# Kernel tuning notes

Hardware: AMD Instinct MI355X
Metric: run time of the kernel (lower is better)

Reference implementation:

```python
import jax, jax.numpy as jnp
import numpy as np

EPS = 1e-5


def gcn_conv(x, W, b, src, dst, ew, num_nodes):
    """GCNConv with add_self_loops=True, symmetric normalization (PyG default)."""
    # degree at destination, self-loop weight 1.0 included implicitly
    deg = jax.ops.segment_sum(ew, dst, num_segments=num_nodes) + 1.0  # [N]
    dinv = jax.lax.rsqrt(deg)                                         # deg >= 1
    norm = dinv[src] * ew * dinv[dst]                                 # [E]
    h = x @ W                                                         # [N, F]
    msg = norm[:, None] * h[src]                                      # [E, F]
    agg = jax.ops.segment_sum(msg, dst, num_segments=num_nodes)       # [N, F]
    # self-loop contribution: dinv[i] * 1 * dinv[i] = 1/deg[i]
    agg = agg + h * (1.0 / deg)[:, None]
    return agg + b


def batchnorm(h, gamma, beta):
    mean = jnp.mean(h, axis=0)
    var = jnp.mean(jnp.square(h - mean), axis=0)  # biased, training-mode stats
    return (h - mean) * jax.lax.rsqrt(var + EPS) * gamma + beta


def setup_inputs() -> dict:
    key = jax.random.key(0)
    ks = jax.random.split(key, 8)
    N, E, F = 50000, 800000, 64
    x = jax.random.normal(ks[0], (N, F), dtype=jnp.float32)
    edge_index = jax.random.randint(ks[1], (2, E), 0, N, dtype=jnp.int64)
    edge_weight = jax.random.uniform(ks[2], (E,), dtype=jnp.float32)
    s = 1.0 / np.sqrt(F)
    W1 = jax.random.uniform(ks[3], (F, F), jnp.float32, -s, s)
    b1 = jnp.zeros((F,), jnp.float32)
    W2 = jax.random.uniform(ks[4], (F, F), jnp.float32, -s, s)
    b2 = jnp.zeros((F,), jnp.float32)
    gamma1 = jnp.ones((F,), jnp.float32)
    beta1 = jnp.zeros((F,), jnp.float32)
    gamma2 = jnp.ones((F,), jnp.float32)
    beta2 = jnp.zeros((F,), jnp.float32)
    return {"x": x, "edge_index": edge_index, "edge_weight": edge_weight,
            "W1": W1, "b1": b1, "gamma1": gamma1, "beta1": beta1,
            "W2": W2, "b2": b2, "gamma2": gamma2, "beta2": beta2}


def reference(x, edge_index, edge_weight, W1, b1, gamma1, beta1, W2, b2, gamma2, beta2):
    N = x.shape[0]
    src, dst = edge_index[0], edge_index[1]
    identity = x
    out = gcn_conv(x, W1, b1, src, dst, edge_weight, N)
    out = jax.nn.relu(batchnorm(out, gamma1, beta1))
    out = gcn_conv(out, W2, b2, src, dst, edge_weight, N)
    out = batchnorm(out, gamma2, beta2)
    out = out + identity  # residual: num_input_features == hidden_dim
    return jax.nn.relu(out)
```

## Files before the change

### kernel.cpp

```cpp
#include <hip/hip_runtime.h>
#include <math.h>

#define FEAT 64
#define BN_EPS 1e-5f

__device__ __forceinline__ int edge_idx(const void* p, int is64, long long i) {
    return is64 ? (int)((const long long*)p)[i] : ((const int*)p)[i];
}

__device__ __forceinline__ float4 f4fma(float a, float4 b, float4 c) {
    return make_float4(fmaf(a, b.x, c.x), fmaf(a, b.y, c.y),
                       fmaf(a, b.z, c.z), fmaf(a, b.w, c.w));
}

__device__ __forceinline__ unsigned bf16rtne(float f) {
    unsigned u = __float_as_uint(f);
    return (u + 0x7fffu + ((u >> 16) & 1u)) >> 16;
}
__device__ __forceinline__ unsigned packbf2(float a, float b) {
    return bf16rtne(a) | (bf16rtne(b) << 16);
}
__device__ __forceinline__ float4 unpackbf4(uint2 r) {
    return make_float4(__uint_as_float(r.x << 16),
                       __uint_as_float(r.x & 0xffff0000u),
                       __uint_as_float(r.y << 16),
                       __uint_as_float(r.y & 0xffff0000u));
}

__global__ __launch_bounds__(256) void init_kernel(
    const unsigned* __restrict__ w, int* __restrict__ flag,
    int* __restrict__ cnt, float* __restrict__ parts, int N) {
    int i = blockIdx.x * 256 + threadIdx.x;
    if (i < N) cnt[i] = 0;
    if (blockIdx.x < 8) parts[blockIdx.x * 256 + threadIdx.x] = 0.0f;
    if (blockIdx.x == 0 && threadIdx.x < 64) {
        unsigned long long ok = __ballot(w[2 * threadIdx.x + 1] == 0u);
        if (threadIdx.x == 0) *flag = (ok == ~0ull);
    }
}

__global__ __launch_bounds__(256) void count_seq_kernel(
    const void* __restrict__ ei, const int* __restrict__ flag,
    int* __restrict__ cnt, int* __restrict__ seq, int E) {
    int is64 = *flag;
    int T = gridDim.x * 256;
    int i = blockIdx.x * 256 + threadIdx.x;
#pragma unroll
    for (int u = 0; u < 8; ++u) {
        int e = i + u * T;
        if (e < E) {
            int dst = edge_idx(ei, is64, (long long)E + e);
            seq[e] = atomicAdd(&cnt[dst], 1);
        }
    }
}

__global__ __launch_bounds__(256) void scan1_kernel(const int* __restrict__ cnt,
                                                    int* __restrict__ excl,
                                                    int* __restrict__ bsum, int N) {
    __shared__ int tmp[256];
    int i = blockIdx.x * 256 + threadIdx.x;
    int v = (i < N) ? cnt[i] : 0;
    tmp[threadIdx.x] = v;
    __syncthreads();
    for (int off = 1; off < 256; off <<= 1) {
        int t = (threadIdx.x >= off) ? tmp[threadIdx.x - off] : 0;
        __syncthreads();
        tmp[threadIdx.x] += t;
        __syncthreads();
    }
    if (i < N) excl[i] = tmp[threadIdx.x] - v;
    if (threadIdx.x == 255) bsum[blockIdx.x] = tmp[255];
}

__global__ __launch_bounds__(256) void scan2_kernel(int* __restrict__ bsum, int nb) {
    __shared__ int tmp[256];
    int i = threadIdx.x;
    int v = (i < nb) ? bsum[i] : 0;
    tmp[i] = v;
    __syncthreads();
    for (int off = 1; off < 256; off <<= 1) {
        int t = (i >= off) ? tmp[i - off] : 0;
        __syncthreads();
        tmp[i] += t;
        __syncthreads();
    }
    if (i < nb) bsum[i] = tmp[i] - v;
}

__global__ void scan3_kernel(const int* __restrict__ excl,
                             const int* __restrict__ bsum,
                             int* __restrict__ rowptr, int N, int E) {
    int i = blockIdx.x * 256 + threadIdx.x;
    if (i < N) rowptr[i] = excl[i] + bsum[blockIdx.x];
    if (i == 0) rowptr[N] = E;
}

__global__ __launch_bounds__(256) void scatter_csr_kernel(
    const void* __restrict__ ei, const float* __restrict__ ew,
    const int* __restrict__ flag, const int* __restrict__ rowptr,
    const int* __restrict__ seq, int2* __restrict__ csr, int E) {
    int is64 = *flag;
    int T = gridDim.x * 256;
    int i = blockIdx.x * 256 + threadIdx.x;
#pragma unroll
    for (int u = 0; u < 2; ++u) {
        int e = i + u * T;
        if (e < E) {
            int src = edge_idx(ei, is64, e);
            int dst = edge_idx(ei, is64, (long long)E + e);
            int pos = rowptr[dst] + seq[e];
            csr[pos] = make_int2(src, __float_as_int(ew[e]));
        }
    }
}

__global__ __launch_bounds__(256) void deg_inv_kernel(
    const int* __restrict__ rowptr, const int2* __restrict__ csr,
    float* __restrict__ dinv, float* __restrict__ invdeg, int N) {
    int t = blockIdx.x * 256 + threadIdx.x;
    int n = t >> 3, l = t & 7;
    if (n >= N) return;
    int b = rowptr[n], e = rowptr[n + 1];
    float d = 0.0f;
    for (int k = b + l; k < e; k += 8) d += __int_as_float(csr[k].y);
    d += __shfl_xor(d, 1);
    d += __shfl_xor(d, 2);
    d += __shfl_xor(d, 4);
    if (l == 0) {
        d += 1.0f;
        dinv[n]   = rsqrtf(d);
        invdeg[n] = 1.0f / d;
    }
}

__global__ __launch_bounds__(256) void fold_kernel(int2* __restrict__ csr,
                                                   const float* __restrict__ dinv,
                                                   int E) {
    int T = gridDim.x * 256;
    int i = blockIdx.x * 256 + threadIdx.x;
#pragma unroll
    for (int u = 0; u < 2; ++u) {
        int e = i + u * T;
        if (e < E) {
            int2 v = csr[e];
            csr[e].y = __float_as_int(dinv[v.x] * __int_as_float(v.y));
        }
    }
}

__global__ __launch_bounds__(256) void gemm64_kernel(
    const float* __restrict__ in, const float* __restrict__ W,
    const float* __restrict__ scale, const float* __restrict__ shift,
    uint2* __restrict__ out_bf, int N, int affine) {
    __shared__ float4 Ws4[64][16];
    __shared__ float xs[64][65];
    __shared__ float sA[64], sS[64];
    int tid = threadIdx.x;
    const float4* W4 = (const float4*)W;
    for (int j = tid; j < 1024; j += 256) Ws4[j >> 4][j & 15] = W4[j];
    if (affine && tid < 64) { sA[tid] = scale[tid]; sS[tid] = shift[tid]; }
    __syncthreads();

    int rowBase = blockIdx.x * 64;
    for (int j = tid; j < 1024; j += 256) {
        int r = j >> 4, q = j & 15;
        int row = rowBase + r;
        float4 v = make_float4(0.f, 0.f, 0.f, 0.f);
        if (row < N) {
            v = ((const float4*)in)[(size_t)row * 16 + q];
            if (affine) {
                int c = q * 4;
                v.x = fmaxf(fmaf(v.x, sA[c + 0], sS[c + 0]), 0.f);
                v.y = fmaxf(fmaf(v.y, sA[c + 1], sS[c + 1]), 0.f);
                v.z = fmaxf(fmaf(v.z, sA[c + 2], sS[c + 2]), 0.f);
                v.w = fmaxf(fmaf(v.w, sA[c + 3], sS[c + 3]), 0.f);
            }
        }
        xs[r][q * 4 + 0] = v.x;
        xs[r][q * 4 + 1] = v.y;
        xs[r][q * 4 + 2] = v.z;
        xs[r][q * 4 + 3] = v.w;
    }
    __syncthreads();

    int q = tid & 15, rg = tid >> 4;
    int r0 = rg * 4;
    float4 a0 = make_float4(0.f, 0.f, 0.f, 0.f), a1 = a0, a2 = a0, a3 = a0;
#pragma unroll 4
    for (int k = 0; k < 64; ++k) {
        float4 wv = Ws4[k][q];
        a0 = f4fma(xs[r0 + 0][k], wv, a0);
        a1 = f4fma(xs[r0 + 1][k], wv, a1);
        a2 = f4fma(xs[r0 + 2][k], wv, a2);
        a3 = f4fma(xs[r0 + 3][k], wv, a3);
    }
    int row = rowBase + r0;
    if (row + 0 < N) out_bf[(size_t)(row + 0) * 16 + q] = make_uint2(packbf2(a0.x, a0.y), packbf2(a0.z, a0.w));
    if (row + 1 < N) out_bf[(size_t)(row + 1) * 16 + q] = make_uint2(packbf2(a1.x, a1.y), packbf2(a1.z, a1.w));
    if (row + 2 < N) out_bf[(size_t)(row + 2) * 16 + q] = make_uint2(packbf2(a2.x, a2.y), packbf2(a2.z, a2.w));
    if (row + 3 < N) out_bf[(size_t)(row + 3) * 16 + q] = make_uint2(packbf2(a3.x, a3.y), packbf2(a3.z, a3.w));
}

__global__ __launch_bounds__(256) void gather_agg_kernel(
    const uint2* __restrict__ h2, const int* __restrict__ rowptr,
    const int2* __restrict__ csr, const float* __restrict__ dinv,
    const float* __restrict__ invdeg, const float* __restrict__ bias,
    float* __restrict__ agg, float* __restrict__ parts, int N) {
    int tid = threadIdx.x;
    int wave = tid >> 6, lane = tid & 63;
    int sub = lane >> 4, sl = lane & 15;
    float4 bv = ((const float4*)bias)[sl];
    float4 bnS = make_float4(0.f, 0.f, 0.f, 0.f), bnQ = bnS;

    for (int n = blockIdx.x * 4 + wave; n < N; n += gridDim.x * 4) {
        int beg = rowptr[n], end = rowptr[n + 1];
        float4 accE = make_float4(0.f, 0.f, 0.f, 0.f);
        int k = beg + sub;
        for (; k + 4 < end; k += 8) {
            int2 e0 = csr[k];
            int2 e1 = csr[k + 4];
            float4 h0 = unpackbf4(h2[(size_t)e0.x * 16 + sl]);
            float4 h1 = unpackbf4(h2[(size_t)e1.x * 16 + sl]);
            accE = f4fma(__int_as_float(e0.y), h0, accE);
            accE = f4fma(__int_as_float(e1.y), h1, accE);
        }
        if (k < end) {
            int2 e0 = csr[k];
            float4 h0 = unpackbf4(h2[(size_t)e0.x * 16 + sl]);
            accE = f4fma(__int_as_float(e0.y), h0, accE);
        }
        accE.x += __shfl_xor(accE.x, 16); accE.y += __shfl_xor(accE.y, 16);
        accE.z += __shfl_xor(accE.z, 16); accE.w += __shfl_xor(accE.w, 16);
        accE.x += __shfl_xor(accE.x, 32); accE.y += __shfl_xor(accE.y, 32);
        accE.z += __shfl_xor(accE.z, 32); accE.w += __shfl_xor(accE.w, 32);

        if (sub == 0) {
            float4 self = unpackbf4(h2[(size_t)n * 16 + sl]);
            float4 tot = f4fma(invdeg[n], self, bv);
            tot = f4fma(dinv[n], accE, tot);
            ((float4*)agg)[(size_t)n * 16 + sl] = tot;
            bnS.x += tot.x; bnS.y += tot.y; bnS.z += tot.z; bnS.w += tot.w;
            bnQ.x = fmaf(tot.x, tot.x, bnQ.x); bnQ.y = fmaf(tot.y, tot.y, bnQ.y);
            bnQ.z = fmaf(tot.z, tot.z, bnQ.z); bnQ.w = fmaf(tot.w, tot.w, bnQ.w);
        }
    }

    __shared__ float4 LS[4][16], LQ[4][16];
    if (sub == 0) { LS[wave][sl] = bnS; LQ[wave][sl] = bnQ; }
    __syncthreads();
    if (tid < 16) {
        float4 ts = LS[0][tid], tq = LQ[0][tid];
        for (int i = 1; i < 4; ++i) {
            float4 a = LS[i][tid], b = LQ[i][tid];
            ts.x += a.x; ts.y += a.y; ts.z += a.z; ts.w += a.w;
            tq.x += b.x; tq.y += b.y; tq.z += b.z; tq.w += b.w;
        }
        float* P = parts + (size_t)(blockIdx.x & 7) * 128;
        int c = tid * 4;
        unsafeAtomicAdd(&P[c + 0], ts.x);      unsafeAtomicAdd(&P[c + 1], ts.y);
        unsafeAtomicAdd(&P[c + 2], ts.z);      unsafeAtomicAdd(&P[c + 3], ts.w);
        unsafeAtomicAdd(&P[64 + c + 0], tq.x); unsafeAtomicAdd(&P[64 + c + 1], tq.y);
        unsafeAtomicAdd(&P[64 + c + 2], tq.z); unsafeAtomicAdd(&P[64 + c + 3], tq.w);
    }
}

__global__ void bn_final_kernel(const float* __restrict__ parts,
                                const float* __restrict__ gamma,
                                const float* __restrict__ beta,
                                float* __restrict__ a, float* __restrict__ s,
                                float invN) {
    int c = threadIdx.x;
    if (c < 64) {
        float sm = 0.f, sq = 0.f;
#pragma unroll
        for (int r = 0; r < 8; ++r) {
            sm += parts[r * 128 + c];
            sq += parts[r * 128 + 64 + c];
        }
        float m = sm * invN;
        float var = fmaxf(sq * invN - m * m, 0.0f);
        float aa = gamma[c] * rsqrtf(var + BN_EPS);
        a[c] = aa;
        s[c] = beta[c] - m * aa;
    }
}

__global__ void final_out_kernel(const float* __restrict__ agg,
                                 const float* __restrict__ a,
                                 const float* __restrict__ s,
                                 const float* __restrict__ x,
                                 float* __restrict__ out, int nquads) {
    int gid = blockIdx.x * 256 + threadIdx.x;
    if (gid < nquads) {
        int q = gid & 15;
        float4 av = ((const float4*)a)[q], sv = ((const float4*)s)[q];
        float4 g = ((const float4*)agg)[gid], xv = ((const float4*)x)[gid];
        float4 o;
        o.x = fmaxf(fmaf(g.x, av.x, sv.x) + xv.x, 0.f);
        o.y = fmaxf(fmaf(g.y, av.y, sv.y) + xv.y, 0.f);
        o.z = fmaxf(fmaf(g.z, av.z, sv.z) + xv.z, 0.f);
        o.w = fmaxf(fmaf(g.w, av.w, sv.w) + xv.w, 0.f);
        ((float4*)out)[gid] = o;
    }
}

extern "C" void kernel_launch(void* const* d_in, const int* in_sizes, int n_in,
                              void* d_out, int out_size, void* d_ws, size_t ws_size,
                              hipStream_t stream) {
    const float* x      = (const float*)d_in[0];
    const void*  ei     = d_in[1];
    const float* ew     = (const float*)d_in[2];
    const float* W1     = (const float*)d_in[3];
    const float* b1     = (const float*)d_in[4];
    const float* gamma1 = (const float*)d_in[5];
    const float* beta1  = (const float*)d_in[6];
    const float* W2     = (const float*)d_in[7];
    const float* b2     = (const float*)d_in[8];
    const float* gamma2 = (const float*)d_in[9];
    const float* beta2  = (const float*)d_in[10];
    float* out = (float*)d_out;

    const int N = in_sizes[0] / FEAT;
    const int E = in_sizes[2];

    char* ws = (char*)d_ws;
    size_t off = 0;
    auto alloc = [&](size_t bytes) {
        size_t o = off;
        off += (bytes + 255) & ~(size_t)255;
        return (void*)(ws + o);
    };
    int*   flag   = (int*)  alloc(256);
    int*   cnt    = (int*)  alloc((size_t)N * 4);
    int*   rowptr = (int*)  alloc((size_t)(N + 1) * 4);
    int*   seq    = (int*)  alloc((size_t)E * 4);
    int*   excl   = (int*)  alloc((size_t)N * 4);
    int*   bsum   = (int*)  alloc(256 * 4);
    float* dinv   = (float*)alloc((size_t)N * 4);
    float* invdeg = (float*)alloc((size_t)N * 4);
    float* parts  = (float*)alloc(2 * 8 * 128 * 4);
    float* ab     = (float*)alloc(256 * 4);
    int2*  csr    = (int2*) alloc((size_t)E * 8);
    uint2* h_bf   = (uint2*)alloc((size_t)N * 16 * 8);
    float* agg    = (float*)alloc((size_t)N * FEAT * 4);

    const int nblkN  = (N + 255) / 256;
    const int nblkN8 = (N * 8 + 255) / 256;
    const int nblkE8 = (E + 2047) / 2048;
    const int nblkE2 = (E + 511) / 512;
    const int nblkQ  = (N * 16 + 255) / 256;
    const int nblkG  = (N + 63) / 64;
    const int GATHER_BLKS = 2048;

    init_kernel<<<nblkN, 256, 0, stream>>>((const unsigned*)ei, flag, cnt, parts, N);
    count_seq_kernel<<<nblkE8, 256, 0, stream>>>(ei, flag, cnt, seq, E);
    scan1_kernel<<<nblkN, 256, 0, stream>>>(cnt, excl, bsum, N);
    scan2_kernel<<<1, 256, 0, stream>>>(bsum, nblkN);
    scan3_kernel<<<nblkN, 256, 0, stream>>>(excl, bsum, rowptr, N, E);
    scatter_csr_kernel<<<nblkE2, 256, 0, stream>>>(ei, ew, flag, rowptr, seq, csr, E);
    deg_inv_kernel<<<nblkN8, 256, 0, stream>>>(rowptr, csr, dinv, invdeg, N);
    fold_kernel<<<nblkE2, 256, 0, stream>>>(csr, dinv, E);

    gemm64_kernel<<<nblkG, 256, 0, stream>>>(x, W1, nullptr, nullptr, h_bf, N, 0);
    gather_agg_kernel<<<GATHER_BLKS, 256, 0, stream>>>(h_bf, rowptr, csr, dinv,
                                                       invdeg, b1, agg, parts, N);
    bn_final_kernel<<<1, 64, 0, stream>>>(parts, gamma1, beta1,
                                          ab, ab + 64, 1.0f / (float)N);

    gemm64_kernel<<<nblkG, 256, 0, stream>>>(agg, W2, ab, ab + 64, h_bf, N, 1);
    gather_agg_kernel<<<GATHER_BLKS, 256, 0, stream>>>(h_bf, rowptr, csr, dinv,
                                                       invdeg, b2, agg, parts + 1024, N);
    bn_final_kernel<<<1, 64, 0, stream>>>(parts + 1024, gamma2, beta2,
                                          ab + 128, ab + 192, 1.0f / (float)N);

    final_out_kernel<<<nblkQ, 256, 0, stream>>>(agg, ab + 128, ab + 192, x,
                                                out, N * 16);
}
```

Before: 218.2 us.

## Launch one wave per node in gather and batch four edge loads per sub-group

The gather-aggregate kernel drops its grid-stride loop and launches one wave per node, with N/4 blocks instead of a fixed 2048. Each sub-group now issues four index loads and then four feature gathers before accumulating, to raise memory-level parallelism. The self row, dinv and invdeg loads are hoisted ahead of the edge loop. The BatchNorm partial-sum replicas grow from 8 to 64 to spread out the atomic contention from the larger number of blocks, at the cost of a longer serial reduction in bn_final.

```diff
diff --git a/kernel.cpp b/kernel.cpp
--- a/kernel.cpp
+++ b/kernel.cpp
@@ -3,6 +3,7 @@
 
 #define FEAT 64
 #define BN_EPS 1e-5f
+#define BN_REPS 64
 
 __device__ __forceinline__ int edge_idx(const void* p, int is64, long long i) {
     return is64 ? (int)((const long long*)p)[i] : ((const int*)p)[i];
@@ -32,7 +33,7 @@
     int* __restrict__ cnt, float* __restrict__ parts, int N) {
     int i = blockIdx.x * 256 + threadIdx.x;
     if (i < N) cnt[i] = 0;
-    if (blockIdx.x < 8) parts[blockIdx.x * 256 + threadIdx.x] = 0.0f;
+    if (blockIdx.x < 64) parts[blockIdx.x * 256 + threadIdx.x] = 0.0f;
     if (blockIdx.x == 0 && threadIdx.x < 64) {
         unsigned long long ok = __ballot(w[2 * threadIdx.x + 1] == 0u);
         if (threadIdx.x == 0) *flag = (ok == ~0ull);
@@ -213,22 +214,31 @@
     float4 bv = ((const float4*)bias)[sl];
     float4 bnS = make_float4(0.f, 0.f, 0.f, 0.f), bnQ = bnS;
 
-    for (int n = blockIdx.x * 4 + wave; n < N; n += gridDim.x * 4) {
+    int n = blockIdx.x * 4 + wave;
+    if (n < N) {
         int beg = rowptr[n], end = rowptr[n + 1];
+        uint2 selfr = h2[(size_t)n * 16 + sl];
+        float dn = dinv[n], idg = invdeg[n];
+
         float4 accE = make_float4(0.f, 0.f, 0.f, 0.f);
-        int k = beg + sub;
-        for (; k + 4 < end; k += 8) {
-            int2 e0 = csr[k];
-            int2 e1 = csr[k + 4];
-            float4 h0 = unpackbf4(h2[(size_t)e0.x * 16 + sl]);
-            float4 h1 = unpackbf4(h2[(size_t)e1.x * 16 + sl]);
-            accE = f4fma(__int_as_float(e0.y), h0, accE);
-            accE = f4fma(__int_as_float(e1.y), h1, accE);
-        }
-        if (k < end) {
-            int2 e0 = csr[k];
-            float4 h0 = unpackbf4(h2[(size_t)e0.x * 16 + sl]);
-            accE = f4fma(__int_as_float(e0.y), h0, accE);
+        for (int k = beg; k < end; k += 16) {
+            int srcs[4]; float w[4];
+#pragma unroll
+            for (int j = 0; j < 4; ++j) {
+                int idx = k + sub + 4 * j;
+                if (idx < end) {
+                    int2 ed = csr[idx];
+                    srcs[j] = ed.x; w[j] = __int_as_float(ed.y);
+                } else { srcs[j] = 0; w[j] = 0.f; }
+            }
+            uint2 hr[4];
+#pragma unroll
+            for (int j = 0; j < 4; ++j)
+                hr[j] = (k + sub + 4 * j < end)
+                          ? h2[(size_t)srcs[j] * 16 + sl] : make_uint2(0u, 0u);
+#pragma unroll
+            for (int j = 0; j < 4; ++j)
+                accE = f4fma(w[j], unpackbf4(hr[j]), accE);
         }
         accE.x += __shfl_xor(accE.x, 16); accE.y += __shfl_xor(accE.y, 16);
         accE.z += __shfl_xor(accE.z, 16); accE.w += __shfl_xor(accE.w, 16);
@@ -236,9 +246,9 @@
         accE.z += __shfl_xor(accE.z, 32); accE.w += __shfl_xor(accE.w, 32);
 
         if (sub == 0) {
-            float4 self = unpackbf4(h2[(size_t)n * 16 + sl]);
-            float4 tot = f4fma(invdeg[n], self, bv);
-            tot = f4fma(dinv[n], accE, tot);
+            float4 self = unpackbf4(selfr);
+            float4 tot = f4fma(idg, self, bv);
+            tot = f4fma(dn, accE, tot);
             ((float4*)agg)[(size_t)n * 16 + sl] = tot;
             bnS.x += tot.x; bnS.y += tot.y; bnS.z += tot.z; bnS.w += tot.w;
             bnQ.x = fmaf(tot.x, tot.x, bnQ.x); bnQ.y = fmaf(tot.y, tot.y, bnQ.y);
@@ -256,7 +266,7 @@
             ts.x += a.x; ts.y += a.y; ts.z += a.z; ts.w += a.w;
             tq.x += b.x; tq.y += b.y; tq.z += b.z; tq.w += b.w;
         }
-        float* P = parts + (size_t)(blockIdx.x & 7) * 128;
+        float* P = parts + (size_t)(blockIdx.x & (BN_REPS - 1)) * 128;
         int c = tid * 4;
         unsafeAtomicAdd(&P[c + 0], ts.x);      unsafeAtomicAdd(&P[c + 1], ts.y);
         unsafeAtomicAdd(&P[c + 2], ts.z);      unsafeAtomicAdd(&P[c + 3], ts.w);
@@ -273,8 +283,7 @@
     int c = threadIdx.x;
     if (c < 64) {
         float sm = 0.f, sq = 0.f;
-#pragma unroll
-        for (int r = 0; r < 8; ++r) {
+        for (int r = 0; r < BN_REPS; ++r) {
             sm += parts[r * 128 + c];
             sq += parts[r * 128 + 64 + c];
         }
@@ -339,7 +348,7 @@
     int*   bsum   = (int*)  alloc(256 * 4);
     float* dinv   = (float*)alloc((size_t)N * 4);
     float* invdeg = (float*)alloc((size_t)N * 4);
-    float* parts  = (float*)alloc(2 * 8 * 128 * 4);
+    float* parts  = (float*)alloc(2 * BN_REPS * 128 * 4);
     float* ab     = (float*)alloc(256 * 4);
     int2*  csr    = (int2*) alloc((size_t)E * 8);
     uint2* h_bf   = (uint2*)alloc((size_t)N * 16 * 8);
@@ -351,7 +360,7 @@
     const int nblkE2 = (E + 511) / 512;
     const int nblkQ  = (N * 16 + 255) / 256;
     const int nblkG  = (N + 63) / 64;
-    const int GATHER_BLKS = 2048;
+    const int nblkA  = (N + 3) / 4;
 
     init_kernel<<<nblkN, 256, 0, stream>>>((const unsigned*)ei, flag, cnt, parts, N);
     count_seq_kernel<<<nblkE8, 256, 0, stream>>>(ei, flag, cnt, seq, E);
@@ -363,15 +372,16 @@
     fold_kernel<<<nblkE2, 256, 0, stream>>>(csr, dinv, E);
 
     gemm64_kernel<<<nblkG, 256, 0, stream>>>(x, W1, nullptr, nullptr, h_bf, N, 0);
-    gather_agg_kernel<<<GATHER_BLKS, 256, 0, stream>>>(h_bf, rowptr, csr, dinv,
-                                                       invdeg, b1, agg, parts, N);
+    gather_agg_kernel<<<nblkA, 256, 0, stream>>>(h_bf, rowptr, csr, dinv,
+                                                 invdeg, b1, agg, parts, N);
     bn_final_kernel<<<1, 64, 0, stream>>>(parts, gamma1, beta1,
                                           ab, ab + 64, 1.0f / (float)N);
 
     gemm64_kernel<<<nblkG, 256, 0, stream>>>(agg, W2, ab, ab + 64, h_bf, N, 1);
-    gather_agg_kernel<<<GATHER_BLKS, 256, 0, stream>>>(h_bf, rowptr, csr, dinv,
-                                                       invdeg, b2, agg, parts + 1024, N);
-    bn_final_kernel<<<1, 64, 0, stream>>>(parts + 1024, gamma2, beta2,
+    gather_agg_kernel<<<nblkA, 256, 0, stream>>>(h_bf, rowptr, csr, dinv,
+                                                 invdeg, b2, agg,
+                                                 parts + BN_REPS * 128, N);
+    bn_final_kernel<<<1, 64, 0, stream>>>(parts + BN_REPS * 128, gamma2, beta2,
                                           ab + 128, ab + 192, 1.0f / (float)N);
 
     final_out_kernel<<<nblkQ, 256, 0, stream>>>(agg, ab + 128, ab + 192, x,
```

After: 208.6 us. 4.4% less time.
